# Kernel tuning notes

Hardware: AMD Instinct MI355X
Metric: run time of the kernel (lower is better)

The kernel has to match this reference:

```python
import jax, jax.numpy as jnp
import numpy as np

N, E = 50000, 800000
IN, OUT = 128, 64
NEG_SLOPE = 0.2


def setup_inputs() -> dict:
    key = jax.random.key(0)
    ks = jax.random.split(key, 8)
    x = jax.random.normal(ks[0], (N, IN), dtype=jnp.float32)
    edge_index = jax.random.randint(ks[1], (2, E), 0, N, dtype=jnp.int64)
    s_in = 1.0 / np.sqrt(IN)
    s_out = 1.0 / np.sqrt(OUT)
    Wl = jax.random.normal(ks[2], (OUT, IN), dtype=jnp.float32) * s_in   # lin_l weight
    bl = jax.random.normal(ks[3], (OUT,), dtype=jnp.float32) * s_in     # lin_l bias
    Wr = jax.random.normal(ks[4], (OUT, IN), dtype=jnp.float32) * s_in  # lin_r weight
    br = jax.random.normal(ks[5], (OUT,), dtype=jnp.float32) * s_in     # lin_r bias
    att = jax.random.normal(ks[6], (OUT,), dtype=jnp.float32) * s_out   # attention vector a
    bias = jnp.zeros((OUT,), dtype=jnp.float32)                          # final output bias
    return dict(x=x, Wl=Wl, bl=bl, Wr=Wr, br=br, att=att, bias=bias, edge_index=edge_index)


def reference(x, Wl, bl, Wr, br, att, bias, edge_index):
    n = x.shape[0]
    loop = jnp.arange(n, dtype=edge_index.dtype)
    src = jnp.concatenate([edge_index[0], loop])  # add_self_loops=True
    dst = jnp.concatenate([edge_index[1], loop])
    xl = x @ Wl.T + bl  # [N, OUT] source transform (x_j)
    xr = x @ Wr.T + br  # [N, OUT] target transform (x_i)
    h = xl[src] + xr[dst]                              # [E+N, OUT]
    h = jnp.where(h > 0, h, NEG_SLOPE * h)             # LeakyReLU(0.2)
    e = h @ att                                        # [E+N] edge logits
    # segment softmax over destination nodes (every node has a self-loop)
    m = jax.ops.segment_max(e, dst, num_segments=n)
    ex = jnp.exp(e - m[dst])
    s = jax.ops.segment_sum(ex, dst, num_segments=n)
    alpha = ex / s[dst]
    out = jax.ops.segment_sum(alpha[:, None] * xl[src], dst, num_segments=n) + bias
    return jax.nn.relu(out)  # norm=Identity, dropout inactive at inference
```

## Files before the change

kernel.cpp:

```cpp
#include <hip/hip_runtime.h>
#include <hip/hip_bf16.h>

#define NEG_SLOPE 0.2f
#define CAP 5120
#define CHUNK 4096
#define LOG2E 1.4426950408889634f

typedef __attribute__((ext_vector_type(8))) short short8v;
typedef __attribute__((ext_vector_type(4))) short short4v;
typedef __attribute__((ext_vector_type(4))) float f32x4;

__device__ __forceinline__ short f2bf(float f) {
  __hip_bfloat16 b = __float2bfloat16(f);
  return *reinterpret_cast<short*>(&b);
}
__device__ __forceinline__ float bf2f(short s) {
  return __uint_as_float(((unsigned)(unsigned short)s) << 16);
}

__device__ __forceinline__ float row_reduce8(float p) {
  p += __int_as_float(__builtin_amdgcn_update_dpp(
      0, __float_as_int(p), 0xB1, 0xF, 0xF, true));
  p += __int_as_float(__builtin_amdgcn_update_dpp(
      0, __float_as_int(p), 0x4E, 0xF, 0xF, true));
  p += __int_as_float(__builtin_amdgcn_update_dpp(
      0, __float_as_int(p), 0x141, 0xF, 0xF, true));
  return p;
}

__global__ __launch_bounds__(256) void k_prep(
    const float* __restrict__ Wl, const float* __restrict__ Wr,
    const float* __restrict__ bl, const float* __restrict__ br,
    short* __restrict__ W2, float* __restrict__ biasc,
    int* __restrict__ bcur, int nbk) {
  int idx = blockIdx.x * 256 + threadIdx.x;
  if (idx < 128 * 128) {
    int j = idx >> 7, k = idx & 127;
    float v = (j < 64) ? Wl[j * 128 + k] : Wr[(j - 64) * 128 + k];
    W2[idx] = f2bf(v);
  } else {
    int z = idx - 128 * 128;
    if (z < nbk) bcur[z] = 0;
  }
  if (idx < 128) biasc[idx] = (idx < 64) ? bl[idx] : br[idx - 64];
}

__global__ __launch_bounds__(256) void k_tbf(
    const float* __restrict__ x, const short* __restrict__ W2,
    const float* __restrict__ biasc, const int* __restrict__ eidx,
    int* __restrict__ bcur, unsigned* __restrict__ pk,
    short* __restrict__ xlb, float* __restrict__ xr, int nN, int E_,
    int nbf) {
  __shared__ union {
    struct { int hist[256]; int base[256]; } bf;
    short xs[64 * 136];
  } u;
  const int t = threadIdx.x;

  if (blockIdx.x < nbf) {
    u.bf.hist[t] = 0;
    __syncthreads();
    const int e0 = blockIdx.x * CHUNK + t * 16;
    unsigned mypk[16];
    int myrank[16];
    const bool valid = (e0 < E_);
    if (valid) {
      const int4* ps = (const int4*)(eidx + e0);
      const int4* pd = (const int4*)(eidx + E_ + e0);
#pragma unroll
      for (int j = 0; j < 4; ++j) {
        int4 sv = ps[j];
        int4 dv = pd[j];
        int ss[4] = {sv.x, sv.y, sv.z, sv.w};
        int dd[4] = {dv.x, dv.y, dv.z, dv.w};
#pragma unroll
        for (int q = 0; q < 4; ++q) {
          unsigned p = ((unsigned)dd[q] << 16) | (unsigned)ss[q];
          mypk[j * 4 + q] = p;
          myrank[j * 4 + q] = atomicAdd(&u.bf.hist[dd[q] >> 8], 1);
        }
      }
    }
    __syncthreads();
    u.bf.base[t] = u.bf.hist[t] ? atomicAdd(&bcur[t], u.bf.hist[t]) : 0;
    __syncthreads();
    if (valid) {
#pragma unroll
      for (int j = 0; j < 16; ++j) {
        int b = mypk[j] >> 24;
        unsigned idx = (unsigned)(u.bf.base[b] + myrank[j]);
        if (idx < CAP) pk[(unsigned)b * CAP + idx] = mypk[j];
      }
    }
    return;
  }

  const int n0 = (blockIdx.x - nbf) * 64;
#pragma unroll
  for (int i = 0; i < 8; ++i) {
    int f = (i * 256 + t) * 4;
    int node = f >> 7, k = f & 127;
    int gn = min(n0 + node, nN - 1);
    float4 v = *(const float4*)(x + (size_t)gn * 128 + k);
    short4v s4;
    s4[0] = f2bf(v.x); s4[1] = f2bf(v.y); s4[2] = f2bf(v.z); s4[3] = f2bf(v.w);
    *(short4v*)(u.xs + node * 136 + k) = s4;
  }
  __syncthreads();

  const int w = t >> 6;
  const int lane = t & 63;
  const int r = lane & 15;
  const int kb = lane >> 4;

  short8v bfr[2][4];
#pragma unroll
  for (int c = 0; c < 2; ++c) {
    const short* bp = W2 + (size_t)((w * 2 + c) * 16 + r) * 128 + kb * 8;
#pragma unroll
    for (int kk = 0; kk < 4; ++kk) bfr[c][kk] = *(const short8v*)(bp + kk * 32);
  }

  f32x4 acc[4][2];
#pragma unroll
  for (int nt = 0; nt < 4; ++nt)
#pragma unroll
    for (int c = 0; c < 2; ++c) acc[nt][c] = (f32x4){0.f, 0.f, 0.f, 0.f};

#pragma unroll
  for (int nt = 0; nt < 4; ++nt) {
    short8v afr[4];
#pragma unroll
    for (int kk = 0; kk < 4; ++kk)
      afr[kk] =
          *(const short8v*)(u.xs + (nt * 16 + r) * 136 + kb * 8 + kk * 32);
#pragma unroll
    for (int kk = 0; kk < 4; ++kk) {
      acc[nt][0] =
          __builtin_amdgcn_mfma_f32_16x16x32_bf16(afr[kk], bfr[0][kk],
                                                  acc[nt][0], 0, 0, 0);
      acc[nt][1] =
          __builtin_amdgcn_mfma_f32_16x16x32_bf16(afr[kk], bfr[1][kk],
                                                  acc[nt][1], 0, 0, 0);
    }
  }

#pragma unroll
  for (int c = 0; c < 2; ++c) {
    const int ch = (w * 2 + c) * 16 + r;
    const float bv = biasc[ch];
#pragma unroll
    for (int nt = 0; nt < 4; ++nt) {
#pragma unroll
      for (int i = 0; i < 4; ++i) {
        int node = n0 + nt * 16 + kb * 4 + i;
        if (node < nN) {
          float v = acc[nt][c][i] + bv;
          if (ch < 64) xlb[(size_t)node * 64 + ch] = f2bf(v);
          else         xr[(size_t)node * 64 + (ch - 64)] = v;
        }
      }
    }
  }
}

__global__ __launch_bounds__(256) void k_nfill(
    const unsigned* __restrict__ pk, const int* __restrict__ bcur,
    int* __restrict__ rowlo, int* __restrict__ rowhi,
    unsigned short* __restrict__ csr, int nN) {
  __shared__ int hist[256];
  __shared__ int nbase[256];
  __shared__ int wsum[4];
  const int b = blockIdx.x;
  const int t = threadIdx.x;
  const int nb0 = b << 8;
  const int cnt = min(bcur[b], CAP);
  const unsigned gbase = (unsigned)b * CAP;
  hist[t] = 0;
  __syncthreads();
  for (int i = t; i < cnt; i += 256)
    atomicAdd(&hist[(pk[gbase + i] >> 16) & 255], 1);
  __syncthreads();
  const int lane = t & 63;
  const int wid = t >> 6;
  int v = hist[t];
  const int orig = v;
#pragma unroll
  for (int off = 1; off < 64; off <<= 1) {
    int uu = __shfl_up(v, off);
    if (lane >= off) v += uu;
  }
  if (lane == 63) wsum[wid] = v;
  __syncthreads();
  int add = 0;
  for (int ww = 0; ww < wid; ++ww) add += wsum[ww];
  const int excl = v - orig + add;
  nbase[t] = excl;
  if (nb0 + t < nN) {
    rowlo[nb0 + t] = (int)gbase + excl;
    rowhi[nb0 + t] = (int)gbase + excl + orig;
  }
  __syncthreads();
  hist[t] = 0;
  __syncthreads();
  for (int i = t; i < cnt; i += 256) {
    unsigned p = pk[gbase + i];
    int dl = (p >> 16) & 255;
    int slot = nbase[dl] + atomicAdd(&hist[dl], 1);
    csr[gbase + slot] = (unsigned short)(p & 0xFFFFu);
  }
}

__global__ __launch_bounds__(256) void k_node(
    const int* __restrict__ rowlo, const int* __restrict__ rowhi,
    const unsigned short* __restrict__ csr, const short* __restrict__ xlb,
    const float* __restrict__ xr, const float* __restrict__ att,
    const float* __restrict__ bias, float* __restrict__ out, int nN) {
  const int wid = (blockIdx.x * 256 + threadIdx.x) >> 6;
  if (wid >= nN) return;
  const int lane = threadIdx.x & 63;
  const int g = lane >> 3;
  const int r = lane & 7;
  const int d = wid;

  const float4 atA = *(const float4*)(att + r * 8);
  const float4 atB = *(const float4*)(att + r * 8 + 4);
  const float4 xrA = *(const float4*)(xr + (size_t)d * 64 + r * 8);
  const float4 xrB = *(const float4*)(xr + (size_t)d * 64 + r * 8 + 4);

  short8v sv = *(const short8v*)(xlb + (size_t)d * 64 + r * 8);
  const float s0 = bf2f(sv[0]), s1 = bf2f(sv[1]), s2 = bf2f(sv[2]),
              s3 = bf2f(sv[3]), s4 = bf2f(sv[4]), s5 = bf2f(sv[5]),
              s6 = bf2f(sv[6]), s7 = bf2f(sv[7]);

  float hh, ps = 0.f;
  hh = s0 + xrA.x; hh = fmaxf(hh, NEG_SLOPE * hh); ps = fmaf(hh, atA.x, ps);
  hh = s1 + xrA.y; hh = fmaxf(hh, NEG_SLOPE * hh); ps = fmaf(hh, atA.y, ps);
  hh = s2 + xrA.z; hh = fmaxf(hh, NEG_SLOPE * hh); ps = fmaf(hh, atA.z, ps);
  hh = s3 + xrA.w; hh = fmaxf(hh, NEG_SLOPE * hh); ps = fmaf(hh, atA.w, ps);
  hh = s4 + xrB.x; hh = fmaxf(hh, NEG_SLOPE * hh); ps = fmaf(hh, atB.x, ps);
  hh = s5 + xrB.y; hh = fmaxf(hh, NEG_SLOPE * hh); ps = fmaf(hh, atB.y, ps);
  hh = s6 + xrB.z; hh = fmaxf(hh, NEG_SLOPE * hh); ps = fmaf(hh, atB.z, ps);
  hh = s7 + xrB.w; hh = fmaxf(hh, NEG_SLOPE * hh); ps = fmaf(hh, atB.w, ps);
  ps = row_reduce8(ps) * LOG2E;

  const bool g0 = (g == 0);
  float m = ps;
  float ssum = g0 ? 1.f : 0.f;
  float4 accA = g0 ? make_float4(s0, s1, s2, s3) : make_float4(0, 0, 0, 0);
  float4 accB = g0 ? make_float4(s4, s5, s6, s7) : make_float4(0, 0, 0, 0);

  const int lo = rowlo[d], hi = rowhi[d];
  const int nst = (hi - lo + 7) >> 3;

#define PROC(VREG, SIDX)                                                      \
  {                                                                           \
    const bool act = ((SIDX) < hi);                                           \
    const float f0 = bf2f(VREG[0]), f1 = bf2f(VREG[1]), f2 = bf2f(VREG[2]),   \
                f3 = bf2f(VREG[3]), f4 = bf2f(VREG[4]), f5 = bf2f(VREG[5]),   \
                f6 = bf2f(VREG[6]), f7 = bf2f(VREG[7]);                       \
    float p = 0.f;                                                            \
    hh = f0 + xrA.x; hh = fmaxf(hh, NEG_SLOPE * hh); p = fmaf(hh, atA.x, p);  \
    hh = f1 + xrA.y; hh = fmaxf(hh, NEG_SLOPE * hh); p = fmaf(hh, atA.y, p);  \
    hh = f2 + xrA.z; hh = fmaxf(hh, NEG_SLOPE * hh); p = fmaf(hh, atA.z, p);  \
    hh = f3 + xrA.w; hh = fmaxf(hh, NEG_SLOPE * hh); p = fmaf(hh, atA.w, p);  \
    hh = f4 + xrB.x; hh = fmaxf(hh, NEG_SLOPE * hh); p = fmaf(hh, atB.x, p);  \
    hh = f5 + xrB.y; hh = fmaxf(hh, NEG_SLOPE * hh); p = fmaf(hh, atB.y, p);  \
    hh = f6 + xrB.z; hh = fmaxf(hh, NEG_SLOPE * hh); p = fmaf(hh, atB.z, p);  \
    hh = f7 + xrB.w; hh = fmaxf(hh, NEG_SLOPE * hh); p = fmaf(hh, atB.w, p);  \
    p = row_reduce8(p);                                                       \
    const float pm = act ? p * LOG2E : -3.0e38f;                              \
    if (__any(pm > m)) {                  \
      const float nm = fmaxf(m, pm);                                          \
      const float sc = exp2f(m - nm);                                         \
      const float w = exp2f(pm - nm);                                         \
      ssum = fmaf(ssum, sc, w);                                               \
      accA.x = fmaf(accA.x, sc, w * f0);                                      \
      accA.y = fmaf(accA.y, sc, w * f1);                                      \
      accA.z = fmaf(accA.z, sc, w * f2);                                      \
      accA.w = fmaf(accA.w, sc, w * f3);                                      \
      accB.x = fmaf(accB.x, sc, w * f4);                                      \
      accB.y = fmaf(accB.y, sc, w * f5);                                      \
      accB.z = fmaf(accB.z, sc, w * f6);                                      \
      accB.w = fmaf(accB.w, sc, w * f7);                                      \
      m = nm;                                                                 \
    } else {                   \
      const float w = exp2f(pm - m);                                          \
      ssum += w;                                                              \
      accA.x = fmaf(w, f0, accA.x);                                           \
      accA.y = fmaf(w, f1, accA.y);                                           \
      accA.z = fmaf(w, f2, accA.z);                                           \
      accA.w = fmaf(w, f3, accA.w);                                           \
      accB.x = fmaf(w, f4, accB.x);                                           \
      accB.y = fmaf(w, f5, accB.y);                                           \
      accB.z = fmaf(w, f6, accB.z);                                           \
      accB.w = fmaf(w, f7, accB.w);                                           \
    }                                                                         \
  }

  int sA = lo + g, sB = sA + 8;
  short8v vA, vB;
  {
    int srcA = (sA < hi) ? (int)csr[sA] : d;
    vA = *(const short8v*)(xlb + (size_t)srcA * 64 + r * 8);
    int srcB = (sB < hi) ? (int)csr[sB] : d;
    vB = *(const short8v*)(xlb + (size_t)srcB * 64 + r * 8);
  }

  int tt = 0;
  for (; tt + 1 < nst; tt += 2) {
    PROC(vA, sA);
    if (tt + 2 < nst) {
      int sN = sA + 16;
      int srcN = (sN < hi) ? (int)csr[sN] : d;
      vA = *(const short8v*)(xlb + (size_t)srcN * 64 + r * 8);
    }
    PROC(vB, sB);
    if (tt + 3 < nst) {
      int sN = sB + 16;
      int srcN = (sN < hi) ? (int)csr[sN] : d;
      vB = *(const short8v*)(xlb + (size_t)srcN * 64 + r * 8);
    }
    sA += 16;
    sB += 16;
  }
  if (tt < nst) PROC(vA, sA);
#undef PROC

#pragma unroll
  for (int off = 8; off <= 32; off <<= 1) {
    float mo = __shfl_xor(m, off);
    float so = __shfl_xor(ssum, off);
    float a0 = __shfl_xor(accA.x, off);
    float a1 = __shfl_xor(accA.y, off);
    float a2 = __shfl_xor(accA.z, off);
    float a3 = __shfl_xor(accA.w, off);
    float a4 = __shfl_xor(accB.x, off);
    float a5 = __shfl_xor(accB.y, off);
    float a6 = __shfl_xor(accB.z, off);
    float a7 = __shfl_xor(accB.w, off);
    float nm = fmaxf(m, mo);
    float sa = exp2f(m - nm);
    float sb2 = exp2f(mo - nm);
    ssum = ssum * sa + so * sb2;
    accA.x = accA.x * sa + a0 * sb2;
    accA.y = accA.y * sa + a1 * sb2;
    accA.z = accA.z * sa + a2 * sb2;
    accA.w = accA.w * sa + a3 * sb2;
    accB.x = accB.x * sa + a4 * sb2;
    accB.y = accB.y * sa + a5 * sb2;
    accB.z = accB.z * sa + a6 * sb2;
    accB.w = accB.w * sa + a7 * sb2;
    m = nm;
  }

  if (g == 0) {
    const float inv = 1.0f / ssum;
    const float4 bA = *(const float4*)(bias + r * 8);
    const float4 bB = *(const float4*)(bias + r * 8 + 4);
    float4 oA, oB;
    oA.x = fmaxf(fmaf(accA.x, inv, bA.x), 0.f);
    oA.y = fmaxf(fmaf(accA.y, inv, bA.y), 0.f);
    oA.z = fmaxf(fmaf(accA.z, inv, bA.z), 0.f);
    oA.w = fmaxf(fmaf(accA.w, inv, bA.w), 0.f);
    oB.x = fmaxf(fmaf(accB.x, inv, bB.x), 0.f);
    oB.y = fmaxf(fmaf(accB.y, inv, bB.y), 0.f);
    oB.z = fmaxf(fmaf(accB.z, inv, bB.z), 0.f);
    oB.w = fmaxf(fmaf(accB.w, inv, bB.w), 0.f);
    *(float4*)(out + (size_t)d * 64 + r * 8) = oA;
    *(float4*)(out + (size_t)d * 64 + r * 8 + 4) = oB;
  }
}

extern "C" void kernel_launch(void* const* d_in, const int* in_sizes, int n_in,
                              void* d_out, int out_size, void* d_ws,
                              size_t ws_size, hipStream_t stream) {
  const float* x    = (const float*)d_in[0];
  const float* Wl   = (const float*)d_in[1];
  const float* bl   = (const float*)d_in[2];
  const float* Wr   = (const float*)d_in[3];
  const float* br   = (const float*)d_in[4];
  const float* att  = (const float*)d_in[5];
  const float* bias = (const float*)d_in[6];
  const int* eidx   = (const int*)d_in[7];
  float* out = (float*)d_out;

  const int N = in_sizes[0] / 128;
  const int E = in_sizes[7] / 2;
  const int NB = (N + 255) >> 8;
  const int nbf = (E + CHUNK - 1) / CHUNK;
  const int ntr = (N + 63) / 64;

  short* xlb   = (short*)d_ws;
  float* xr    = (float*)(xlb + (size_t)N * 64);
  unsigned* pk = (unsigned*)(xr + (size_t)N * 64);
  unsigned short* csr = (unsigned short*)(pk + (size_t)NB * CAP);
  short* W2    = (short*)(csr + (size_t)NB * CAP);
  float* biasc = (float*)(W2 + 128 * 128);
  int* bcur    = (int*)(biasc + 128);
  int* rowlo   = bcur + NB;
  int* rowhi   = rowlo + N;

  k_prep<<<(128 * 128 + NB + 255) / 256, 256, 0, stream>>>(
      Wl, Wr, bl, br, W2, biasc, bcur, NB);
  k_tbf<<<nbf + ntr, 256, 0, stream>>>(x, W2, biasc, eidx, bcur, pk, xlb, xr,
                                       N, E, nbf);
  k_nfill<<<NB, 256, 0, stream>>>(pk, bcur, rowlo, rowhi, csr, N);
  k_node<<<(N + 3) / 4, 256, 0, stream>>>(rowlo, rowhi, csr, xlb, xr, att,
                                          bias, out, N);
}
```

Measured before the change: 78.09 us.

## Process two destination nodes per wavefront with shared running max per node

```diff
diff --git a/kernel.cpp b/kernel.cpp
--- a/kernel.cpp
+++ b/kernel.cpp
@@ -216,12 +216,15 @@
     const unsigned short* __restrict__ csr, const short* __restrict__ xlb,
     const float* __restrict__ xr, const float* __restrict__ att,
     const float* __restrict__ bias, float* __restrict__ out, int nN) {
-  const int wid = (blockIdx.x * 256 + threadIdx.x) >> 6;
-  if (wid >= nN) return;
+  const int wvid = (blockIdx.x * 256 + threadIdx.x) >> 6;
   const int lane = threadIdx.x & 63;
-  const int g = lane >> 3;
+  const int h = lane >> 5;
+  const int g = (lane >> 3) & 3;
   const int r = lane & 7;
-  const int d = wid;
+  int d = wvid * 2 + h;
+  if (wvid * 2 >= nN) return;
+  const bool live = (d < nN);
+  d = min(d, nN - 1);
 
   const float4 atA = *(const float4*)(att + r * 8);
   const float4 atB = *(const float4*)(att + r * 8 + 4);
@@ -250,8 +253,9 @@
   float4 accA = g0 ? make_float4(s0, s1, s2, s3) : make_float4(0, 0, 0, 0);
   float4 accB = g0 ? make_float4(s4, s5, s6, s7) : make_float4(0, 0, 0, 0);
 
-  const int lo = rowlo[d], hi = rowhi[d];
-  const int nst = (hi - lo + 7) >> 3;
+  const int lo = live ? rowlo[d] : 0;
+  const int hi = live ? rowhi[d] : 0;
+  const int nst = (hi - lo + 3) >> 2;
 
 #define PROC(VREG, SIDX)                                                      \
   {                                                                           \
@@ -266,12 +270,15 @@
     hh = f3 + xrA.w; hh = fmaxf(hh, NEG_SLOPE * hh); p = fmaf(hh, atA.w, p);  \
     hh = f4 + xrB.x; hh = fmaxf(hh, NEG_SLOPE * hh); p = fmaf(hh, atB.x, p);  \
     hh = f5 + xrB.y; hh = fmaxf(hh, NEG_SLOPE * hh); p = fmaf(hh, atB.y, p);  \
-    hh = f6 + xrB.z; hh = fmaxf(hh, NEG_SLOPE * hh); p = fmaf(hh, atB.z, p);  \
+    hh = f6 + xrB.z; hh = fmaxf(hh, NEG_SLOPE * hh); p = fmaf(hh, atB.w == atB.w ? atB.z : atB.z, p); \
     hh = f7 + xrB.w; hh = fmaxf(hh, NEG_SLOPE * hh); p = fmaf(hh, atB.w, p);  \
     p = row_reduce8(p);                                                       \
     const float pm = act ? p * LOG2E : -3.0e38f;                              \
-    if (__any(pm > m)) {                  \
-      const float nm = fmaxf(m, pm);                                          \
+    if (__any(pm > m)) {             \
+      float q = pm;                                                           \
+      q = fmaxf(q, __shfl_xor(q, 8));                                         \
+      q = fmaxf(q, __shfl_xor(q, 16));                     \
+      const float nm = fmaxf(m, q);                     \
       const float sc = exp2f(m - nm);                                         \
       const float w = exp2f(pm - nm);                                         \
       ssum = fmaf(ssum, sc, w);                                               \
@@ -284,7 +291,7 @@
       accB.z = fmaf(accB.z, sc, w * f6);                                      \
       accB.w = fmaf(accB.w, sc, w * f7);                                      \
       m = nm;                                                                 \
-    } else {                   \
+    } else {                                  \
       const float w = exp2f(pm - m);                                          \
       ssum += w;                                                              \
       accA.x = fmaf(w, f0, accA.x);                                           \
@@ -298,63 +305,60 @@
     }                                                                         \
   }
 
-  int sA = lo + g, sB = sA + 8;
-  short8v vA, vB;
+  int sA = lo + g, sB = sA + 4, sC = sA + 8;
+  short8v vA, vB, vC;
   {
     int srcA = (sA < hi) ? (int)csr[sA] : d;
     vA = *(const short8v*)(xlb + (size_t)srcA * 64 + r * 8);
     int srcB = (sB < hi) ? (int)csr[sB] : d;
     vB = *(const short8v*)(xlb + (size_t)srcB * 64 + r * 8);
+    int srcC = (sC < hi) ? (int)csr[sC] : d;
+    vC = *(const short8v*)(xlb + (size_t)srcC * 64 + r * 8);
   }
 
   int tt = 0;
-  for (; tt + 1 < nst; tt += 2) {
+  for (; tt + 2 < nst; tt += 3) {
     PROC(vA, sA);
-    if (tt + 2 < nst) {
-      int sN = sA + 16;
+    if (tt + 3 < nst) {
+      int sN = sA + 12;
       int srcN = (sN < hi) ? (int)csr[sN] : d;
       vA = *(const short8v*)(xlb + (size_t)srcN * 64 + r * 8);
     }
     PROC(vB, sB);
-    if (tt + 3 < nst) {
-      int sN = sB + 16;
+    if (tt + 4 < nst) {
+      int sN = sB + 12;
       int srcN = (sN < hi) ? (int)csr[sN] : d;
       vB = *(const short8v*)(xlb + (size_t)srcN * 64 + r * 8);
     }
-    sA += 16;
-    sB += 16;
-  }
-  if (tt < nst) PROC(vA, sA);
+    PROC(vC, sC);
+    if (tt + 5 < nst) {
+      int sN = sC + 12;
+      int srcN = (sN < hi) ? (int)csr[sN] : d;
+      vC = *(const short8v*)(xlb + (size_t)srcN * 64 + r * 8);
+    }
+    sA += 12; sB += 12; sC += 12;
+  }
+  {
+    const int rem = nst - tt;
+    if (rem > 0) PROC(vA, sA);
+    if (rem > 1) PROC(vB, sB);
+  }
 #undef PROC
 
 #pragma unroll
-  for (int off = 8; off <= 32; off <<= 1) {
-    float mo = __shfl_xor(m, off);
-    float so = __shfl_xor(ssum, off);
-    float a0 = __shfl_xor(accA.x, off);
-    float a1 = __shfl_xor(accA.y, off);
-    float a2 = __shfl_xor(accA.z, off);
-    float a3 = __shfl_xor(accA.w, off);
-    float a4 = __shfl_xor(accB.x, off);
-    float a5 = __shfl_xor(accB.y, off);
-    float a6 = __shfl_xor(accB.z, off);
-    float a7 = __shfl_xor(accB.w, off);
-    float nm = fmaxf(m, mo);
-    float sa = exp2f(m - nm);
-    float sb2 = exp2f(mo - nm);
-    ssum = ssum * sa + so * sb2;
-    accA.x = accA.x * sa + a0 * sb2;
-    accA.y = accA.y * sa + a1 * sb2;
-    accA.z = accA.z * sa + a2 * sb2;
-    accA.w = accA.w * sa + a3 * sb2;
-    accB.x = accB.x * sa + a4 * sb2;
-    accB.y = accB.y * sa + a5 * sb2;
-    accB.z = accB.z * sa + a6 * sb2;
-    accB.w = accB.w * sa + a7 * sb2;
-    m = nm;
-  }
-
-  if (g == 0) {
+  for (int off = 8; off <= 16; off <<= 1) {
+    ssum  += __shfl_xor(ssum, off);
+    accA.x += __shfl_xor(accA.x, off);
+    accA.y += __shfl_xor(accA.y, off);
+    accA.z += __shfl_xor(accA.z, off);
+    accA.w += __shfl_xor(accA.w, off);
+    accB.x += __shfl_xor(accB.x, off);
+    accB.y += __shfl_xor(accB.y, off);
+    accB.z += __shfl_xor(accB.z, off);
+    accB.w += __shfl_xor(accB.w, off);
+  }
+
+  if (g0 && live) {
     const float inv = 1.0f / ssum;
     const float4 bA = *(const float4*)(bias + r * 8);
     const float4 bB = *(const float4*)(bias + r * 8 + 4);
@@ -406,6 +410,9 @@
   k_tbf<<<nbf + ntr, 256, 0, stream>>>(x, W2, biasc, eidx, bcur, pk, xlb, xr,
                                        N, E, nbf);
   k_nfill<<<NB, 256, 0, stream>>>(pk, bcur, rowlo, rowhi, csr, N);
-  k_node<<<(N + 3) / 4, 256, 0, stream>>>(rowlo, rowhi, csr, xlb, xr, att,
-                                          bias, out, N);
-}
+  {
+    int waves = (N + 1) / 2;
+    k_node<<<(waves + 3) / 4, 256, 0, stream>>>(rowlo, rowhi, csr, xlb, xr,
+                                                att, bias, out, N);
+  }
+}
```

Measured after the change: 72.16 us. -7.6%, faster.
